# Optimization experiments

Measured on AMD Instinct MI355X. Metric: run time of the kernel, lower is better.

The kernel has to match this reference:

```python
import jax, jax.numpy as jnp
import numpy as np

NB_CLASSES = 1024
SZ_EMBED = 128
N_SAMPLES = 262144
MRG = 0.1
ALPHA = 32.0


def l2_norm(x):
    # matches torch l2_norm: divide by sqrt(sum(x^2, dim=1) + 1e-12)
    return x / jnp.sqrt(jnp.sum(x * x, axis=1, keepdims=True) + 1e-12)


def setup_inputs() -> dict:
    key = jax.random.key(0)
    k1, k2, k3 = jax.random.split(key, 3)
    X = jax.random.normal(k1, (N_SAMPLES, SZ_EMBED), dtype=jnp.float32)
    proxies = jax.random.normal(k2, (NB_CLASSES, SZ_EMBED), dtype=jnp.float32)
    T = jax.random.randint(k3, (N_SAMPLES,), 0, NB_CLASSES)
    return {"X": X, "proxies": proxies, "T": T}


def reference(X, proxies, T):
    # cosine similarities: [N, C]
    cos = l2_norm(X) @ l2_norm(proxies).T
    # on-device one-hot replaces the numpy binarize roundtrip
    P_one_hot = jax.nn.one_hot(T, NB_CLASSES, dtype=cos.dtype)  # [N, C]
    pos_exp_w = jnp.exp(-ALPHA * (cos - MRG)) * P_one_hot
    neg_exp_w = jnp.exp(ALPHA * (cos + MRG)) * (1.0 - P_one_hot)
    P_sim_sum = pos_exp_w.sum(axis=0)  # [C]
    N_sim_sum = neg_exp_w.sum(axis=0)  # [C]
    num_valid = (P_one_hot.sum(axis=0) != 0).sum().astype(cos.dtype)
    pos_term = jnp.where(
        num_valid > 0,
        jnp.log1p(P_sim_sum).sum() / jnp.maximum(num_valid, 1.0),
        jnp.zeros((), cos.dtype),
    )
    neg_term = jnp.log1p(N_sim_sum).sum() / NB_CLASSES
    loss = pos_term + neg_term
    return jnp.stack([loss, pos_term, neg_term])
```

## Files before the change

### kernel.cpp

```cpp
#include <hip/hip_runtime.h>
#include <math.h>

#define NB_CLASSES 1024
#define SZ_EMBED 128
#define N_SAMPLES 262144
#define MTILE 64
#define CTILE 64
#define NBLOCKS (N_SAMPLES / MTILE)
#define XSTRIDE 136

typedef __bf16 v8bf __attribute__((ext_vector_type(8)));
typedef float v4f __attribute__((ext_vector_type(4)));

#define EXP_A 46.16624130844683f
#define EXP_B 4.616624130844683f

#define SMEM_BYTES 19712

__device__ __forceinline__ unsigned short f2bf(float f) {
    union { float f; unsigned u; } v; v.f = f;
    unsigned u = v.u;
    unsigned rounding = 0x7FFFu + ((u >> 16) & 1u);
    return (unsigned short)((u + rounding) >> 16);
}
__device__ __forceinline__ float bfbits_lo(unsigned u) {
    union { unsigned u; float f; } v; v.u = u << 16; return v.f;
}
__device__ __forceinline__ float bfbits_hi(unsigned u) {
    union { unsigned u; float f; } v; v.u = u & 0xffff0000u; return v.f;
}

__global__ __launch_bounds__(256) void norm_proxies_kernel(
    const float* __restrict__ proxies, unsigned short* __restrict__ pn) {
    int wv = threadIdx.x >> 6;
    int lane = threadIdx.x & 63;
    int row = blockIdx.x * 4 + wv;
    const float* src = proxies + (size_t)row * SZ_EMBED + lane * 2;
    float2 x = *(const float2*)src;
    float ss = x.x * x.x + x.y * x.y;
    #pragma unroll
    for (int off = 32; off; off >>= 1) ss += __shfl_xor(ss, off);
    float inv = rsqrtf(ss + 1e-12f);
    unsigned pk = (unsigned)f2bf(x.x * inv) | ((unsigned)f2bf(x.y * inv) << 16);
    *(unsigned*)(pn + (size_t)row * SZ_EMBED + lane * 2) = pk;
}

__global__ __launch_bounds__(256, 4) void main_kernel(
    const float* __restrict__ X, const int* __restrict__ T,
    const unsigned short* __restrict__ Pn,
    float* __restrict__ partial_neg, float* __restrict__ partial_pos) {
    __shared__ __align__(16) char smem[SMEM_BYTES];
    unsigned short* xtile = (unsigned short*)smem;
    float (*psum)[4] = (float(*)[4])(smem + 17408);
    float (*dsum)[4] = (float(*)[4])(smem + 18432);
    int* tT = (int*)(smem + 19456);
    float* neg_lds = (float*)smem;
    float* pos_lds = (float*)(smem + 4096);

    const int t = threadIdx.x;
    const int lane = t & 63;
    const int wv = t >> 6;
    const int quad = lane >> 4;
    const int l15 = lane & 15;
    const int sample_base = blockIdx.x * MTILE;

    const int row = t >> 2, part = t & 3;
    {
        const float4* src = (const float4*)(X + (size_t)(sample_base + row) * SZ_EMBED + part * 32);
        float4 r[8];
        float ss = 0.f;
        #pragma unroll
        for (int j = 0; j < 8; ++j) {
            r[j] = src[j];
            ss += r[j].x * r[j].x + r[j].y * r[j].y + r[j].z * r[j].z + r[j].w * r[j].w;
        }
        psum[row][part] = ss;
        if (t < MTILE) tT[t] = T[sample_base + t];
        __syncthreads();
        float inv = rsqrtf(psum[row][0] + psum[row][1] + psum[row][2] + psum[row][3] + 1e-12f);
        unsigned short* dst = xtile + row * XSTRIDE + part * 32;
        #pragma unroll
        for (int j = 0; j < 8; ++j) {
            uint2 pk;
            pk.x = (unsigned)f2bf(r[j].x * inv) | ((unsigned)f2bf(r[j].y * inv) << 16);
            pk.y = (unsigned)f2bf(r[j].z * inv) | ((unsigned)f2bf(r[j].w * inv) << 16);
            *(uint2*)(dst + j * 4) = pk;
        }
        int lbl = tT[row];
        const unsigned short* prow = Pn + (size_t)lbl * SZ_EMBED + part * 32;
        float d = 0.f;
        #pragma unroll
        for (int j = 0; j < 4; ++j) {
            uint4 pv = *(const uint4*)(prow + j * 8);
            float4 xa = r[2 * j], xb = r[2 * j + 1];
            d += bfbits_lo(pv.x) * xa.x + bfbits_hi(pv.x) * xa.y;
            d += bfbits_lo(pv.y) * xa.z + bfbits_hi(pv.y) * xa.w;
            d += bfbits_lo(pv.z) * xb.x + bfbits_hi(pv.z) * xb.y;
            d += bfbits_lo(pv.w) * xb.z + bfbits_hi(pv.w) * xb.w;
        }
        dsum[row][part] = d * inv;
    }
    __syncthreads();

    v8bf afrag[4][4];
    #pragma unroll
    for (int ri = 0; ri < 4; ++ri)
        #pragma unroll
        for (int kc = 0; kc < 4; ++kc)
            afrag[ri][kc] = *(const v8bf*)(xtile + (ri * 16 + l15) * XSTRIDE + kc * 32 + quad * 8);

    float diag_pos = 0.f, diag_neg = 0.f;
    int diag_lbl = 0;
    if (part == 0) {
        diag_lbl = tT[row];
        float dd = dsum[row][0] + dsum[row][1] + dsum[row][2] + dsum[row][3];
        diag_pos = __builtin_amdgcn_exp2f(fmaf(dd, -EXP_A, EXP_B));
        diag_neg = __builtin_amdgcn_exp2f(fmaf(dd,  EXP_A, EXP_B));
    }
    __syncthreads();

    *(float4*)(neg_lds + 4 * t) = float4{0.f, 0.f, 0.f, 0.f};
    *(float4*)(pos_lds + 4 * t) = float4{0.f, 0.f, 0.f, 0.f};
    __syncthreads();

    if (part == 0) {
        atomicAdd(&pos_lds[diag_lbl], diag_pos);
        atomicAdd(&neg_lds[diag_lbl], -diag_neg);
    }

    const unsigned short* bptr = Pn + (size_t)(wv * 16 + l15) * SZ_EMBED + quad * 8;
    v8bf bfrag[4];
    #pragma unroll
    for (int kc = 0; kc < 4; ++kc)
        bfrag[kc] = *(const v8bf*)(bptr + kc * 32);

    for (int ct = 0; ct < NB_CLASSES / CTILE; ++ct) {
        v4f zero = {0.f, 0.f, 0.f, 0.f};
        v4f acc[4] = {zero, zero, zero, zero};
        #pragma unroll
        for (int kc = 0; kc < 4; ++kc)
            #pragma unroll
            for (int ri = 0; ri < 4; ++ri)
                acc[ri] = __builtin_amdgcn_mfma_f32_16x16x32_bf16(afrag[ri][kc], bfrag[kc], acc[ri], 0, 0, 0);

        if (ct < NB_CLASSES / CTILE - 1) {
            const unsigned short* nb = bptr + (size_t)(ct + 1) * CTILE * SZ_EMBED;
            #pragma unroll
            for (int kc = 0; kc < 4; ++kc)
                bfrag[kc] = *(const v8bf*)(nb + kc * 32);
        }

        float e[16];
        #pragma unroll
        for (int ri = 0; ri < 4; ++ri)
            #pragma unroll
            for (int r = 0; r < 4; ++r)
                e[ri * 4 + r] = __builtin_amdgcn_exp2f(fmaf(acc[ri][r], EXP_A, EXP_B));
        #pragma unroll
        for (int s = 8; s; s >>= 1)
            #pragma unroll
            for (int j = 0; j < s; ++j)
                e[j] += e[j + s];
        atomicAdd(&neg_lds[ct * CTILE + wv * 16 + l15], e[0]);
    }
    __syncthreads();

    float* nrow = partial_neg + (size_t)blockIdx.x * NB_CLASSES;
    float* prow = partial_pos + (size_t)blockIdx.x * NB_CLASSES;
    *(float4*)(nrow + 4 * t) = *(const float4*)(neg_lds + 4 * t);
    *(float4*)(prow + 4 * t) = *(const float4*)(pos_lds + 4 * t);
}

__global__ __launch_bounds__(256) void row_reduce_kernel(
    float* __restrict__ partial_neg, float* __restrict__ partial_pos) {
    const int t = threadIdx.x;
    const size_t base = (size_t)blockIdx.x * 64 * NB_CLASSES;
    float4 an = {0.f, 0.f, 0.f, 0.f}, ap = {0.f, 0.f, 0.f, 0.f};
    for (int r = 0; r < 64; ++r) {
        const float* nrow = partial_neg + base + (size_t)r * NB_CLASSES;
        const float* prow = partial_pos + base + (size_t)r * NB_CLASSES;
        float4 vn = *(const float4*)(nrow + 4 * t);
        float4 vp = *(const float4*)(prow + 4 * t);
        an.x += vn.x; an.y += vn.y; an.z += vn.z; an.w += vn.w;
        ap.x += vp.x; ap.y += vp.y; ap.z += vp.z; ap.w += vp.w;
    }
    *(float4*)(partial_neg + base + 4 * t) = an;
    *(float4*)(partial_pos + base + 4 * t) = ap;
}

__global__ __launch_bounds__(256) void finalize_kernel(
    const float* __restrict__ partial_neg, const float* __restrict__ partial_pos,
    float* __restrict__ out) {
    int t = threadIdx.x;
    float4 ns = {0.f, 0.f, 0.f, 0.f}, ps = {0.f, 0.f, 0.f, 0.f};
    #pragma unroll 8
    for (int r = 0; r < 64; ++r) {
        float4 vn = *(const float4*)(partial_neg + (size_t)r * 64 * NB_CLASSES + 4 * t);
        float4 vp = *(const float4*)(partial_pos + (size_t)r * 64 * NB_CLASSES + 4 * t);
        ns.x += vn.x; ns.y += vn.y; ns.z += vn.z; ns.w += vn.w;
        ps.x += vp.x; ps.y += vp.y; ps.z += vp.z; ps.w += vp.w;
    }
    float lp_pos = log1pf(ps.x) + log1pf(ps.y) + log1pf(ps.z) + log1pf(ps.w);
    float lp_neg = log1pf(ns.x) + log1pf(ns.y) + log1pf(ns.z) + log1pf(ns.w);
    float valid = (ps.x != 0.f) + (ps.y != 0.f) + (ps.z != 0.f) + (ps.w != 0.f);
    #pragma unroll
    for (int off = 32; off; off >>= 1) {
        lp_pos += __shfl_xor(lp_pos, off);
        lp_neg += __shfl_xor(lp_neg, off);
        valid  += __shfl_xor(valid, off);
    }
    __shared__ float s[3][4];
    int wv = t >> 6, lane = t & 63;
    if (lane == 0) { s[0][wv] = lp_pos; s[1][wv] = lp_neg; s[2][wv] = valid; }
    __syncthreads();
    if (t == 0) {
        float P = s[0][0] + s[0][1] + s[0][2] + s[0][3];
        float Ng = s[1][0] + s[1][1] + s[1][2] + s[1][3];
        float V = s[2][0] + s[2][1] + s[2][2] + s[2][3];
        float pos_term = (V > 0.f) ? (P / fmaxf(V, 1.f)) : 0.f;
        float neg_term = Ng / (float)NB_CLASSES;
        out[0] = pos_term + neg_term;
        out[1] = pos_term;
        out[2] = neg_term;
    }
}

extern "C" void kernel_launch(void* const* d_in, const int* in_sizes, int n_in,
                              void* d_out, int out_size, void* d_ws, size_t ws_size,
                              hipStream_t stream) {
    const float* X = (const float*)d_in[0];
    const float* proxies = (const float*)d_in[1];
    const int* T = (const int*)d_in[2];
    float* out = (float*)d_out;

    char* ws = (char*)d_ws;
    unsigned short* Pn = (unsigned short*)ws;
    float* partial_neg = (float*)(ws + (size_t)NB_CLASSES * SZ_EMBED * sizeof(unsigned short));
    float* partial_pos = partial_neg + (size_t)NBLOCKS * NB_CLASSES;

    norm_proxies_kernel<<<NB_CLASSES / 4, 256, 0, stream>>>(proxies, Pn);
    main_kernel<<<NBLOCKS, 256, 0, stream>>>(X, T, Pn, partial_neg, partial_pos);
    row_reduce_kernel<<<64, 256, 0, stream>>>(partial_neg, partial_pos);
    finalize_kernel<<<1, 256, 0, stream>>>(partial_neg, partial_pos, out);
}
```

Baseline: 311.0 us.

## Accumulate diagonal terms globally and keep per-block class sums in registers

The positive and diagonal-negative terms now go straight into two small global arrays via atomics, which removes the per-block partial_pos buffer and halves the partial-sum traffic. Negative-exp sums are held in registers across two row groups, with double-buffered proxy fragments, and written once per block after cross-quad shuffles, replacing LDS atomics and the zeroing and sync steps. The row reduce is split across more blocks, and a memset is added to clear the global accumulators. The costs are global atomic contention on the label bins, re-reading the proxy tiles twice per block, and float atomics that make the sum order nondeterministic.

```diff
diff --git a/kernel.cpp b/kernel.cpp
--- a/kernel.cpp
+++ b/kernel.cpp
@@ -48,14 +48,13 @@
 __global__ __launch_bounds__(256, 4) void main_kernel(
     const float* __restrict__ X, const int* __restrict__ T,
     const unsigned short* __restrict__ Pn,
-    float* __restrict__ partial_neg, float* __restrict__ partial_pos) {
+    float* __restrict__ partial_neg, float* __restrict__ pos_g,
+    float* __restrict__ negd_g) {
     __shared__ __align__(16) char smem[SMEM_BYTES];
     unsigned short* xtile = (unsigned short*)smem;
     float (*psum)[4] = (float(*)[4])(smem + 17408);
     float (*dsum)[4] = (float(*)[4])(smem + 18432);
     int* tT = (int*)(smem + 19456);
-    float* neg_lds = (float*)smem;
-    float* pos_lds = (float*)(smem + 4096);
 
     const int t = threadIdx.x;
     const int lane = t & 63;
@@ -63,8 +62,8 @@
     const int quad = lane >> 4;
     const int l15 = lane & 15;
     const int sample_base = blockIdx.x * MTILE;
-
     const int row = t >> 2, part = t & 3;
+
     {
         const float4* src = (const float4*)(X + (size_t)(sample_base + row) * SZ_EMBED + part * 32);
         float4 r[8];
@@ -99,107 +98,96 @@
             d += bfbits_lo(pv.w) * xb.z + bfbits_hi(pv.w) * xb.w;
         }
         dsum[row][part] = d * inv;
-    }
-    __syncthreads();
-
-    v8bf afrag[4][4];
-    #pragma unroll
-    for (int ri = 0; ri < 4; ++ri)
-        #pragma unroll
-        for (int kc = 0; kc < 4; ++kc)
-            afrag[ri][kc] = *(const v8bf*)(xtile + (ri * 16 + l15) * XSTRIDE + kc * 32 + quad * 8);
-
-    float diag_pos = 0.f, diag_neg = 0.f;
-    int diag_lbl = 0;
-    if (part == 0) {
-        diag_lbl = tT[row];
-        float dd = dsum[row][0] + dsum[row][1] + dsum[row][2] + dsum[row][3];
-        diag_pos = __builtin_amdgcn_exp2f(fmaf(dd, -EXP_A, EXP_B));
-        diag_neg = __builtin_amdgcn_exp2f(fmaf(dd,  EXP_A, EXP_B));
-    }
-    __syncthreads();
-
-    *(float4*)(neg_lds + 4 * t) = float4{0.f, 0.f, 0.f, 0.f};
-    *(float4*)(pos_lds + 4 * t) = float4{0.f, 0.f, 0.f, 0.f};
-    __syncthreads();
-
-    if (part == 0) {
-        atomicAdd(&pos_lds[diag_lbl], diag_pos);
-        atomicAdd(&neg_lds[diag_lbl], -diag_neg);
+        __syncthreads();
+        if (part == 0) {
+            float dd = dsum[row][0] + dsum[row][1] + dsum[row][2] + dsum[row][3];
+            float dp = __builtin_amdgcn_exp2f(fmaf(dd, -EXP_A, EXP_B));
+            float dn = __builtin_amdgcn_exp2f(fmaf(dd,  EXP_A, EXP_B));
+            atomicAdd(&pos_g[lbl], dp);
+            atomicAdd(&negd_g[lbl], dn);
+        }
     }
 
     const unsigned short* bptr = Pn + (size_t)(wv * 16 + l15) * SZ_EMBED + quad * 8;
-    v8bf bfrag[4];
-    #pragma unroll
-    for (int kc = 0; kc < 4; ++kc)
-        bfrag[kc] = *(const v8bf*)(bptr + kc * 32);
-
-    for (int ct = 0; ct < NB_CLASSES / CTILE; ++ct) {
-        v4f zero = {0.f, 0.f, 0.f, 0.f};
-        v4f acc[4] = {zero, zero, zero, zero};
-        #pragma unroll
-        for (int kc = 0; kc < 4; ++kc)
-            #pragma unroll
-            for (int ri = 0; ri < 4; ++ri)
-                acc[ri] = __builtin_amdgcn_mfma_f32_16x16x32_bf16(afrag[ri][kc], bfrag[kc], acc[ri], 0, 0, 0);
-
-        if (ct < NB_CLASSES / CTILE - 1) {
-            const unsigned short* nb = bptr + (size_t)(ct + 1) * CTILE * SZ_EMBED;
+    float e_acc[16];
+    #pragma unroll
+    for (int ct = 0; ct < 16; ++ct) e_acc[ct] = 0.f;
+
+    #pragma unroll 1
+    for (int rg = 0; rg < 2; ++rg) {
+        v8bf afrag[2][4];
+        #pragma unroll
+        for (int ri = 0; ri < 2; ++ri)
             #pragma unroll
             for (int kc = 0; kc < 4; ++kc)
-                bfrag[kc] = *(const v8bf*)(nb + kc * 32);
-        }
-
-        float e[16];
-        #pragma unroll
-        for (int ri = 0; ri < 4; ++ri)
+                afrag[ri][kc] = *(const v8bf*)(xtile + (rg * 32 + ri * 16 + l15) * XSTRIDE + kc * 32 + quad * 8);
+
+        v8bf bfrag[2][4];
+        #pragma unroll
+        for (int kc = 0; kc < 4; ++kc)
+            bfrag[0][kc] = *(const v8bf*)(bptr + kc * 32);
+
+        #pragma unroll
+        for (int ct = 0; ct < 16; ++ct) {
+            const int cur = ct & 1, nxt = cur ^ 1;
+            if (ct < 15) {
+                const unsigned short* nb = bptr + (size_t)(ct + 1) * CTILE * SZ_EMBED;
+                #pragma unroll
+                for (int kc = 0; kc < 4; ++kc)
+                    bfrag[nxt][kc] = *(const v8bf*)(nb + kc * 32);
+            }
+            v4f zero = {0.f, 0.f, 0.f, 0.f};
+            v4f acc0 = zero, acc1 = zero;
             #pragma unroll
-            for (int r = 0; r < 4; ++r)
-                e[ri * 4 + r] = __builtin_amdgcn_exp2f(fmaf(acc[ri][r], EXP_A, EXP_B));
-        #pragma unroll
-        for (int s = 8; s; s >>= 1)
+            for (int kc = 0; kc < 4; ++kc) {
+                acc0 = __builtin_amdgcn_mfma_f32_16x16x32_bf16(afrag[0][kc], bfrag[cur][kc], acc0, 0, 0, 0);
+                acc1 = __builtin_amdgcn_mfma_f32_16x16x32_bf16(afrag[1][kc], bfrag[cur][kc], acc1, 0, 0, 0);
+            }
+            float e[8];
             #pragma unroll
-            for (int j = 0; j < s; ++j)
-                e[j] += e[j + s];
-        atomicAdd(&neg_lds[ct * CTILE + wv * 16 + l15], e[0]);
-    }
-    __syncthreads();
+            for (int r = 0; r < 4; ++r) {
+                e[r]     = __builtin_amdgcn_exp2f(fmaf(acc0[r], EXP_A, EXP_B));
+                e[4 + r] = __builtin_amdgcn_exp2f(fmaf(acc1[r], EXP_A, EXP_B));
+            }
+            e[0] += e[4]; e[1] += e[5]; e[2] += e[6]; e[3] += e[7];
+            e[0] += e[2]; e[1] += e[3];
+            e_acc[ct] += e[0] + e[1];
+        }
+    }
 
     float* nrow = partial_neg + (size_t)blockIdx.x * NB_CLASSES;
-    float* prow = partial_pos + (size_t)blockIdx.x * NB_CLASSES;
-    *(float4*)(nrow + 4 * t) = *(const float4*)(neg_lds + 4 * t);
-    *(float4*)(prow + 4 * t) = *(const float4*)(pos_lds + 4 * t);
-}
-
-__global__ __launch_bounds__(256) void row_reduce_kernel(
-    float* __restrict__ partial_neg, float* __restrict__ partial_pos) {
+    #pragma unroll
+    for (int ct = 0; ct < 16; ++ct) {
+        float v = e_acc[ct];
+        v += __shfl_xor(v, 16);
+        v += __shfl_xor(v, 32);
+        if (quad == 0) nrow[ct * CTILE + wv * 16 + l15] = v;
+    }
+}
+
+__global__ __launch_bounds__(256) void row_reduce_kernel(float* __restrict__ partial_neg) {
     const int t = threadIdx.x;
-    const size_t base = (size_t)blockIdx.x * 64 * NB_CLASSES;
-    float4 an = {0.f, 0.f, 0.f, 0.f}, ap = {0.f, 0.f, 0.f, 0.f};
-    for (int r = 0; r < 64; ++r) {
-        const float* nrow = partial_neg + base + (size_t)r * NB_CLASSES;
-        const float* prow = partial_pos + base + (size_t)r * NB_CLASSES;
-        float4 vn = *(const float4*)(nrow + 4 * t);
-        float4 vp = *(const float4*)(prow + 4 * t);
-        an.x += vn.x; an.y += vn.y; an.z += vn.z; an.w += vn.w;
-        ap.x += vp.x; ap.y += vp.y; ap.z += vp.z; ap.w += vp.w;
-    }
-    *(float4*)(partial_neg + base + 4 * t) = an;
-    *(float4*)(partial_pos + base + 4 * t) = ap;
+    const int g = blockIdx.x >> 2, q = blockIdx.x & 3;
+    float* base = partial_neg + (size_t)g * 64 * NB_CLASSES + q * 256 + t;
+    float s = 0.f;
+    #pragma unroll 8
+    for (int r = 0; r < 64; ++r) s += base[(size_t)r * NB_CLASSES];
+    base[0] = s;
 }
 
 __global__ __launch_bounds__(256) void finalize_kernel(
-    const float* __restrict__ partial_neg, const float* __restrict__ partial_pos,
-    float* __restrict__ out) {
+    const float* __restrict__ partial_neg, const float* __restrict__ pos_g,
+    const float* __restrict__ negd_g, float* __restrict__ out) {
     int t = threadIdx.x;
-    float4 ns = {0.f, 0.f, 0.f, 0.f}, ps = {0.f, 0.f, 0.f, 0.f};
+    float4 ns = {0.f, 0.f, 0.f, 0.f};
     #pragma unroll 8
     for (int r = 0; r < 64; ++r) {
         float4 vn = *(const float4*)(partial_neg + (size_t)r * 64 * NB_CLASSES + 4 * t);
-        float4 vp = *(const float4*)(partial_pos + (size_t)r * 64 * NB_CLASSES + 4 * t);
         ns.x += vn.x; ns.y += vn.y; ns.z += vn.z; ns.w += vn.w;
-        ps.x += vp.x; ps.y += vp.y; ps.z += vp.z; ps.w += vp.w;
-    }
+    }
+    float4 nd = *(const float4*)(negd_g + 4 * t);
+    ns.x -= nd.x; ns.y -= nd.y; ns.z -= nd.z; ns.w -= nd.w;
+    float4 ps = *(const float4*)(pos_g + 4 * t);
     float lp_pos = log1pf(ps.x) + log1pf(ps.y) + log1pf(ps.z) + log1pf(ps.w);
     float lp_neg = log1pf(ns.x) + log1pf(ns.y) + log1pf(ns.z) + log1pf(ns.w);
     float valid = (ps.x != 0.f) + (ps.y != 0.f) + (ps.z != 0.f) + (ps.w != 0.f);
@@ -235,11 +223,13 @@
 
     char* ws = (char*)d_ws;
     unsigned short* Pn = (unsigned short*)ws;
-    float* partial_neg = (float*)(ws + (size_t)NB_CLASSES * SZ_EMBED * sizeof(unsigned short));
-    float* partial_pos = partial_neg + (size_t)NBLOCKS * NB_CLASSES;
-
+    float* pos_g = (float*)(ws + (size_t)NB_CLASSES * SZ_EMBED * sizeof(unsigned short));
+    float* negd_g = pos_g + NB_CLASSES;
+    float* partial_neg = negd_g + NB_CLASSES;
+
+    hipMemsetAsync(pos_g, 0, 2 * NB_CLASSES * sizeof(float), stream);
     norm_proxies_kernel<<<NB_CLASSES / 4, 256, 0, stream>>>(proxies, Pn);
-    main_kernel<<<NBLOCKS, 256, 0, stream>>>(X, T, Pn, partial_neg, partial_pos);
-    row_reduce_kernel<<<64, 256, 0, stream>>>(partial_neg, partial_pos);
-    finalize_kernel<<<1, 256, 0, stream>>>(partial_neg, partial_pos, out);
-}
+    main_kernel<<<NBLOCKS, 256, 0, stream>>>(X, T, Pn, partial_neg, pos_g, negd_g);
+    row_reduce_kernel<<<256, 256, 0, stream>>>(partial_neg);
+    finalize_kernel<<<1, 256, 0, stream>>>(partial_neg, pos_g, negd_g, out);
+}
```

Measured after the change: 751.0 us. +141.5%, slower.
